# Kernel tuning notes

Measured on AMD Instinct MI355X. Metric: run time of the kernel, lower is better.

The kernel has to match this reference:

```python
import jax, jax.numpy as jnp
import numpy as np

B, N, E, T = 32768, 6, 6, 2  # batch graphs, nodes, edges (ring), edge types
H, DIN = 128, 3


def _ring_rel():
    # off_diag[i, (i+1)%N] = 1 -> edge e: sender i, receiver (i+1)%N
    send = np.arange(N)
    recv = (np.arange(N) + 1) % N
    eye = np.eye(N, dtype=np.float32)
    return jnp.asarray(eye[recv]), jnp.asarray(eye[send])  # rel_rec, rel_send [E,N]


def setup_inputs() -> dict:
    key = jax.random.key(0)
    ks = iter(jax.random.split(key, 40))
    rn = lambda shape, s=0.1: jax.random.normal(next(ks), shape, jnp.float32) * s
    rel_rec, rel_send = _ring_rel()
    inp = {
        'x': rn((B, N, DIN), 1.0),
        'rel_rec': rel_rec, 'rel_send': rel_send,
        'e1w1': rn((DIN, H)), 'e1b1': jnp.full((H,), 0.1), 'e1w2': rn((H, H)), 'e1b2': jnp.full((H,), 0.1),
        'e2w1': rn((2 * H, H)), 'e2b1': jnp.full((H,), 0.1), 'e2w2': rn((H, H)), 'e2b2': jnp.full((H,), 0.1),
        'e3w1': rn((H, H)), 'e3b1': jnp.full((H,), 0.1), 'e3w2': rn((H, H)), 'e3b2': jnp.full((H,), 0.1),
        'e4w1': rn((2 * H, H)), 'e4b1': jnp.full((H,), 0.1), 'e4w2': rn((H, H)), 'e4b2': jnp.full((H,), 0.1),
        'ew_out': rn((H, T)), 'eb_out': jnp.full((T,), 0.1),
        'd_msg_w1': rn((T, 2 * DIN, H)), 'd_msg_b1': rn((T, H), 0.01),
        'd_msg_w2': rn((T, H, H)), 'd_msg_b2': rn((T, H), 0.01),
        'd_out_w1': rn((DIN + H, H)), 'd_out_b1': rn((H,), 0.01),
        'd_out_w2': rn((H, H)), 'd_out_b2': rn((H,), 0.01),
        'd_out_w3': rn((H, DIN)), 'd_out_b3': rn((DIN,), 0.01),
    }
    return inp


def _mlp(h, w1, b1, w2, b2):
    # two-layer ELU MLP (dropout inactive at eval)
    return jax.nn.elu(jax.nn.elu(h @ w1 + b1) @ w2 + b2)


def reference(x, rel_rec, rel_send,
              e1w1, e1b1, e1w2, e1b2, e2w1, e2b1, e2w2, e2b2,
              e3w1, e3b1, e3w2, e3b2, e4w1, e4b1, e4w2, e4b2,
              ew_out, eb_out,
              d_msg_w1, d_msg_b1, d_msg_w2, d_msg_b2,
              d_out_w1, d_out_b1, d_out_w2, d_out_b2, d_out_w3, d_out_b3):
    node2edge = lambda h: jnp.concatenate(
        [jnp.einsum('en,bnh->beh', rel_rec, h), jnp.einsum('en,bnh->beh', rel_send, h)], axis=-1)

    # ---- GraphEncoder (factor=False) ----
    h = _mlp(x, e1w1, e1b1, e1w2, e1b2)                      # [B,N,H]
    he = _mlp(node2edge(h), e2w1, e2b1, e2w2, e2b2)          # [B,E,H]
    h2 = _mlp(he, e3w1, e3b1, e3w2, e3b2)                    # [B,E,H]
    h3 = _mlp(jnp.concatenate([h2, he], -1), e4w1, e4b1, e4w2, e4b2)
    logits = h3 @ ew_out + eb_out                            # [B,E,T]
    rel_type = jax.nn.softmax(logits, axis=-1)               # edge-type weights

    # ---- GraphDecoder single step (skip_first=False) ----
    recv = jnp.einsum('en,bnd->bed', rel_rec, x)             # [B,E,DIN]
    send = jnp.einsum('en,bnd->bed', rel_send, x)
    pre_msg = jnp.concatenate([recv, send], axis=-1)         # [B,E,2*DIN]
    # batched per-edge-type MLP: one grouped GEMM instead of a python loop of layers
    m = jax.nn.relu(jnp.einsum('bei,tih->bteh', pre_msg, d_msg_w1) + d_msg_b1[None, :, None, :])
    m = jax.nn.relu(jnp.einsum('bteh,tho->bteo', m, d_msg_w2) + d_msg_b2[None, :, None, :])
    all_msgs = jnp.einsum('bteh,bet->beh', m, rel_type)      # weight + accumulate over types
    agg_msgs = jnp.einsum('beh,en->bnh', all_msgs, rel_rec)  # edge -> node aggregation

    aug = jnp.concatenate([x, agg_msgs], axis=-1)            # [B,N,DIN+H]
    p = jax.nn.relu(aug @ d_out_w1 + d_out_b1)
    p = jax.nn.relu(p @ d_out_w2 + d_out_b2)
    p = p @ d_out_w3 + d_out_b3
    return x + p                                             # [B,N,DIN]
```

## Files before the change

kernel.cpp:

```cpp
#include <hip/hip_runtime.h>
#include <hip/hip_bf16.h>

typedef __bf16 bf16x8 __attribute__((ext_vector_type(8)));
typedef float floatx4 __attribute__((ext_vector_type(4)));

#define LDW 136
#define PXW 40

#define O_E1W2  0
#define O_E2W1  16384
#define O_E2W2  49152
#define O_E3W1  65536
#define O_E3W2  81920
#define O_E4W1  98304
#define O_E4W2  131072
#define O_DM2T0 147456
#define O_DM2T1 163840
#define O_DO1   180224
#define O_DO2   196608
#define O_EWOUT 212992
#define O_DW3   215040
#define O_E1W1P 217088
#define O_M1T0P 221184
#define O_M1T1P 225280
#define O_DO1XP 229376
#define WS_ELEMS 233472

__global__ void prep_kernel(const float* e1w2, const float* e2w1, const float* e2w2,
    const float* e3w1, const float* e3w2, const float* e4w1, const float* e4w2,
    const float* dmsg2, const float* dout1, const float* dout2,
    const float* ew_out, const float* dout_w3, const float* e1w1,
    const float* dmsg_w1, __hip_bfloat16* ws) {
  int idx = blockIdx.x * 256 + threadIdx.x;
  if (idx >= WS_ELEMS) return;
  float v;
  if (idx < O_E2W1)      { int l = idx;           v = e1w2[(l & 127) * 128 + (l >> 7)]; }
  else if (idx < O_E2W2) { int l = idx - O_E2W1;  v = e2w1[(l & 255) * 128 + (l >> 8)]; }
  else if (idx < O_E3W1) { int l = idx - O_E2W2;  v = e2w2[(l & 127) * 128 + (l >> 7)]; }
  else if (idx < O_E3W2) { int l = idx - O_E3W1;  v = e3w1[(l & 127) * 128 + (l >> 7)]; }
  else if (idx < O_E4W1) { int l = idx - O_E3W2;  v = e3w2[(l & 127) * 128 + (l >> 7)]; }
  else if (idx < O_E4W2) { int l = idx - O_E4W1;  v = e4w1[(l & 255) * 128 + (l >> 8)]; }
  else if (idx < O_DM2T0){ int l = idx - O_E4W2;  v = e4w2[(l & 127) * 128 + (l >> 7)]; }
  else if (idx < O_DM2T1){ int l = idx - O_DM2T0; v = dmsg2[(l & 127) * 128 + (l >> 7)]; }
  else if (idx < O_DO1)  { int l = idx - O_DM2T1; v = dmsg2[16384 + (l & 127) * 128 + (l >> 7)]; }
  else if (idx < O_DO2)  { int l = idx - O_DO1;   v = dout1[384 + (l & 127) * 128 + (l >> 7)]; }
  else if (idx < O_EWOUT){ int l = idx - O_DO2;   v = dout2[(l & 127) * 128 + (l >> 7)]; }
  else if (idx < O_DW3)  { int l = idx - O_EWOUT; int n = l >> 7;
                           v = (n < 2) ? ew_out[(l & 127) * 2 + n] : 0.f; }
  else if (idx < O_E1W1P){ int l = idx - O_DW3;   int n = l >> 7;
                           v = (n < 3) ? dout_w3[(l & 127) * 3 + n] : 0.f; }
  else if (idx < O_M1T0P){ int l = idx - O_E1W1P; int n = l >> 5, c = l & 31;
                           v = (c >= 3 && c < 6) ? e1w1[(c - 3) * 128 + n] : 0.f; }
  else if (idx < O_M1T1P){ int l = idx - O_M1T0P; int n = l >> 5, c = l & 31;
                           v = (c < 6) ? dmsg_w1[c * 128 + n] : 0.f; }
  else if (idx < O_DO1XP){ int l = idx - O_M1T1P; int n = l >> 5, c = l & 31;
                           v = (c < 6) ? dmsg_w1[768 + c * 128 + n] : 0.f; }
  else                   { int l = idx - O_DO1XP; int n = l >> 5, c = l & 31;
                           v = (c >= 3 && c < 6) ? dout1[(c - 3) * 128 + n] : 0.f; }
  ws[idx] = __float2bfloat16(v);
}

__global__ __launch_bounds__(512, 4) void nri_fused(
    const float* __restrict__ x,
    const float* __restrict__ e1b1, const float* __restrict__ e1b2,
    const float* __restrict__ e2b1, const float* __restrict__ e2b2,
    const float* __restrict__ e3b1, const float* __restrict__ e3b2,
    const float* __restrict__ e4b1, const float* __restrict__ e4b2,
    const float* __restrict__ eb_out,
    const float* __restrict__ dmsg_b1, const float* __restrict__ dmsg_b2,
    const float* __restrict__ dout_b1, const float* __restrict__ dout_b2,
    const float* __restrict__ dout_b3,
    const __bf16* __restrict__ wt, float* __restrict__ out)
{
  const int tid  = threadIdx.x;
  const int wave = tid >> 6;
  const int lane = tid & 63;
  const int nl   = lane & 15;
  const int quad = lane >> 4;
  const int colb = wave * 16 + nl;
  const int gx   = blockIdx.x * 288;

  __shared__ __align__(16) __hip_bfloat16 bufA[96 * LDW];
  __shared__ __align__(16) __hip_bfloat16 bufB[96 * LDW];
  __shared__ __align__(16) __hip_bfloat16 pxb[96 * PXW];
  __shared__ __align__(16) float biasL[16 * 128];
  __shared__ float rtw[192];
  __shared__ float xs[288];
  __shared__ float obuf[288];

  for (int i = tid; i < 288; i += 512) xs[i] = x[gx + i];
  for (int i = tid; i < 2048; i += 512) {
    int row = i >> 7, c = i & 127;
    float v;
    switch (row) {
      case 0: v = e1b1[c]; break;   case 1: v = e1b2[c]; break;
      case 2: v = e2b1[c]; break;   case 3: v = e2b2[c]; break;
      case 4: v = e3b1[c]; break;   case 5: v = e3b2[c]; break;
      case 6: v = e4b1[c]; break;   case 7: v = e4b2[c]; break;
      case 8: v = dmsg_b1[c]; break;  case 9: v = dmsg_b1[128 + c]; break;
      case 10: v = dmsg_b2[c]; break; case 11: v = dmsg_b2[128 + c]; break;
      case 12: v = dout_b1[c]; break; case 13: v = dout_b2[c]; break;
      case 14: v = (c < 2) ? eb_out[c] : 0.f; break;
      default: v = (c < 3) ? dout_b3[c] : 0.f; break;
    }
    biasL[i] = v;
  }
  for (int i = tid; i < 96 * 32; i += 512) {
    int row = i >> 5, c = i & 31;
    int e = row % 6;
    float v = 0.f;
    if (c < 3)      { int rr = row + ((e == 5) ? -5 : 1); v = x[gx + rr * 3 + c]; }
    else if (c < 6) v = x[gx + row * 3 + (c - 3)];
    pxb[row * PXW + c] = __float2bfloat16(v);
  }
  __syncthreads();

  auto initb = [&](floatx4 (&a)[6], int brow) {
    float bv = biasL[brow * 128 + colb];
    floatx4 v = {bv, bv, bv, bv};
#pragma unroll
    for (int mt = 0; mt < 6; ++mt) a[mt] = v;
  };

  auto gemm128 = [&](floatx4 (&acc)[6], const __hip_bfloat16* in, const __bf16* w) {
    const __bf16* ab = (const __bf16*)(const void*)in;
    const __bf16* w0 = w + colb * 128 + quad * 8;
#pragma unroll
    for (int ks = 0; ks < 4; ++ks) {
      int kk = ks * 32 + quad * 8;
      bf16x8 b0 = *(const bf16x8*)(w0 + ks * 32);
#pragma unroll
      for (int mt = 0; mt < 6; ++mt) {
        bf16x8 a = *(const bf16x8*)(ab + (mt * 16 + nl) * LDW + kk);
        acc[mt] = __builtin_amdgcn_mfma_f32_16x16x32_bf16(a, b0, acc[mt], 0, 0, 0);
      }
    }
  };

  auto gemm256 = [&](floatx4 (&acc)[6], const __hip_bfloat16* in0, bool recv0,
                     const __hip_bfloat16* in1, const __bf16* w) {
    int rofs0[6], rofs1[6];
#pragma unroll
    for (int mt = 0; mt < 6; ++mt) {
      int r = mt * 16 + nl;
      rofs1[mt] = r * LDW;
      if (recv0) { int e = r % 6; r += (e == 5) ? -5 : 1; }
      rofs0[mt] = r * LDW;
    }
    const __bf16* ab0 = (const __bf16*)(const void*)in0;
    const __bf16* ab1 = (const __bf16*)(const void*)in1;
    const __bf16* w0 = w + colb * 256 + quad * 8;
#pragma unroll
    for (int ks = 0; ks < 8; ++ks) {
      int kk = (ks & 3) * 32 + quad * 8;
      const __bf16* ab = (ks < 4) ? ab0 : ab1;
      const int* rofs = (ks < 4) ? rofs0 : rofs1;
      bf16x8 b0 = *(const bf16x8*)(w0 + ks * 32);
#pragma unroll
      for (int mt = 0; mt < 6; ++mt) {
        bf16x8 a = *(const bf16x8*)(ab + rofs[mt] + kk);
        acc[mt] = __builtin_amdgcn_mfma_f32_16x16x32_bf16(a, b0, acc[mt], 0, 0, 0);
      }
    }
  };

  auto gemm32 = [&](floatx4 (&acc)[6], int wofs) {
    const __bf16* pb = (const __bf16*)(const void*)pxb;
    bf16x8 b0 = *(const bf16x8*)(wt + wofs + colb * 32 + quad * 8);
#pragma unroll
    for (int mt = 0; mt < 6; ++mt) {
      bf16x8 a = *(const bf16x8*)(pb + (mt * 16 + nl) * PXW + quad * 8);
      acc[mt] = __builtin_amdgcn_mfma_f32_16x16x32_bf16(a, b0, acc[mt], 0, 0, 0);
    }
  };

  auto store_act = [&](floatx4 (&acc)[6], int act, __hip_bfloat16* ob) {
#pragma unroll
    for (int mt = 0; mt < 6; ++mt)
#pragma unroll
      for (int r = 0; r < 4; ++r) {
        float z = acc[mt][r];
        if (act == 1) z = (z > 0.f) ? z : (__expf(z) - 1.f);
        else z = fmaxf(z, 0.f);
        ob[(mt * 16 + quad * 4 + r) * LDW + colb] = __float2bfloat16(z);
      }
  };

  floatx4 acc[6];

  initb(acc, 0); gemm32(acc, O_E1W1P); store_act(acc, 1, bufA);
  __syncthreads();
  initb(acc, 1); gemm128(acc, bufA, wt + O_E1W2); store_act(acc, 1, bufB);
  __syncthreads();
  initb(acc, 2); gemm256(acc, bufB, true, bufB, wt + O_E2W1); store_act(acc, 1, bufA);
  __syncthreads();
  initb(acc, 3); gemm128(acc, bufA, wt + O_E2W2); store_act(acc, 1, bufB);
  __syncthreads();
  initb(acc, 4); gemm128(acc, bufB, wt + O_E3W1); store_act(acc, 1, bufA);
  __syncthreads();
  initb(acc, 5); gemm128(acc, bufA, wt + O_E3W2);
  __syncthreads();
  store_act(acc, 1, bufA);
  __syncthreads();
  initb(acc, 6); gemm256(acc, bufA, false, bufB, wt + O_E4W1);
  __syncthreads();
  store_act(acc, 1, bufA);
  __syncthreads();
  initb(acc, 7); gemm128(acc, bufA, wt + O_E4W2); store_act(acc, 1, bufB);
  __syncthreads();

  if (wave < 6) {
    int tile = wave;
    float bv = biasL[14 * 128 + nl];
    floatx4 lg = {bv, bv, bv, bv};
    const __bf16* ab = (const __bf16*)(const void*)bufB;
    const __bf16* wp = wt + O_EWOUT + nl * 128 + quad * 8;
#pragma unroll
    for (int ks = 0; ks < 4; ++ks) {
      bf16x8 a = *(const bf16x8*)(ab + (tile * 16 + nl) * LDW + ks * 32 + quad * 8);
      bf16x8 b = *(const bf16x8*)(wp + ks * 32);
      lg = __builtin_amdgcn_mfma_f32_16x16x32_bf16(a, b, lg, 0, 0, 0);
    }
    if (nl < 2) {
#pragma unroll
      for (int r = 0; r < 4; ++r)
        rtw[(tile * 16 + quad * 4 + r) * 2 + nl] = lg[r];
    }
  }
  __syncthreads();

  if (tid < 96) {
    float l0 = rtw[tid * 2], l1 = rtw[tid * 2 + 1];
    float mx = fmaxf(l0, l1);
    float ea = __expf(l0 - mx), eb = __expf(l1 - mx);
    float inv = 1.f / (ea + eb);
    rtw[tid * 2] = ea * inv; rtw[tid * 2 + 1] = eb * inv;
  }
  {
    floatx4 acc1[6];
    initb(acc, 8);  gemm32(acc, O_M1T0P);  store_act(acc, 2, bufA);
    initb(acc1, 9); gemm32(acc1, O_M1T1P); store_act(acc1, 2, bufB);
    __syncthreads();

    initb(acc, 10);  gemm128(acc, bufA, wt + O_DM2T0);
    initb(acc1, 11); gemm128(acc1, bufB, wt + O_DM2T1);
#pragma unroll
    for (int mt = 0; mt < 6; ++mt)
#pragma unroll
      for (int r = 0; r < 4; ++r) {
        int row = mt * 16 + quad * 4 + r;
        float r0 = rtw[row * 2], r1 = rtw[row * 2 + 1];
        acc[mt][r] = r0 * fmaxf(acc[mt][r], 0.f) + r1 * fmaxf(acc1[mt][r], 0.f);
      }
  }
  __syncthreads();

#pragma unroll
  for (int mt = 0; mt < 6; ++mt)
#pragma unroll
    for (int r = 0; r < 4; ++r) {
      int row = mt * 16 + quad * 4 + r;
      int e = row % 6;
      int orow = row + ((e == 5) ? -5 : 1);
      bufA[orow * LDW + colb] = __float2bfloat16(acc[mt][r]);
    }
  __syncthreads();

  initb(acc, 12); gemm128(acc, bufA, wt + O_DO1); gemm32(acc, O_DO1XP);
  store_act(acc, 2, bufB);
  __syncthreads();
  initb(acc, 13); gemm128(acc, bufB, wt + O_DO2); store_act(acc, 2, bufA);
  __syncthreads();

  if (wave < 6) {
    int tile = wave;
    float bv = biasL[15 * 128 + nl];
    floatx4 d = {bv, bv, bv, bv};
    const __bf16* ab = (const __bf16*)(const void*)bufA;
    const __bf16* wp = wt + O_DW3 + nl * 128 + quad * 8;
#pragma unroll
    for (int ks = 0; ks < 4; ++ks) {
      bf16x8 a = *(const bf16x8*)(ab + (tile * 16 + nl) * LDW + ks * 32 + quad * 8);
      bf16x8 b = *(const bf16x8*)(wp + ks * 32);
      d = __builtin_amdgcn_mfma_f32_16x16x32_bf16(a, b, d, 0, 0, 0);
    }
    if (nl < 3) {
#pragma unroll
      for (int r = 0; r < 4; ++r) {
        int row = tile * 16 + quad * 4 + r;
        obuf[row * 3 + nl] = xs[row * 3 + nl] + d[r];
      }
    }
  }
  __syncthreads();
  for (int i = tid; i < 288; i += 512) out[gx + i] = obuf[i];
}

extern "C" void kernel_launch(void* const* d_in, const int* in_sizes, int n_in,
                              void* d_out, int out_size, void* d_ws, size_t ws_size,
                              hipStream_t stream) {
  const float* x       = (const float*)d_in[0];
  const float* e1w1    = (const float*)d_in[3];
  const float* e1b1    = (const float*)d_in[4];
  const float* e1w2    = (const float*)d_in[5];
  const float* e1b2    = (const float*)d_in[6];
  const float* e2w1    = (const float*)d_in[7];
  const float* e2b1    = (const float*)d_in[8];
  const float* e2w2    = (const float*)d_in[9];
  const float* e2b2    = (const float*)d_in[10];
  const float* e3w1    = (const float*)d_in[11];
  const float* e3b1    = (const float*)d_in[12];
  const float* e3w2    = (const float*)d_in[13];
  const float* e3b2    = (const float*)d_in[14];
  const float* e4w1    = (const float*)d_in[15];
  const float* e4b1    = (const float*)d_in[16];
  const float* e4w2    = (const float*)d_in[17];
  const float* e4b2    = (const float*)d_in[18];
  const float* ew_out  = (const float*)d_in[19];
  const float* eb_out  = (const float*)d_in[20];
  const float* dmsg_w1 = (const float*)d_in[21];
  const float* dmsg_b1 = (const float*)d_in[22];
  const float* dmsg_w2 = (const float*)d_in[23];
  const float* dmsg_b2 = (const float*)d_in[24];
  const float* dout_w1 = (const float*)d_in[25];
  const float* dout_b1 = (const float*)d_in[26];
  const float* dout_w2 = (const float*)d_in[27];
  const float* dout_b2 = (const float*)d_in[28];
  const float* dout_w3 = (const float*)d_in[29];
  const float* dout_b3 = (const float*)d_in[30];

  prep_kernel<<<(WS_ELEMS + 255) / 256, 256, 0, stream>>>(
      e1w2, e2w1, e2w2, e3w1, e3w2, e4w1, e4w2, dmsg_w2, dout_w1, dout_w2,
      ew_out, dout_w3, e1w1, dmsg_w1, (__hip_bfloat16*)d_ws);

  nri_fused<<<32768 / 16, 512, 0, stream>>>(
      x, e1b1, e1b2, e2b1, e2b2, e3b1, e3b2, e4b1, e4b2, eb_out,
      dmsg_b1, dmsg_b2, dout_b1, dout_b2, dout_b3,
      (const __bf16*)d_ws, (float*)d_out);
}
```

Baseline: 276.7 us.

## Prefetch next-layer weights into registers and split e4w1 GEMM to overlap

Weight fragments for the next layer are loaded from global memory into registers before the current layer's activation store and barrier, so their latency overlaps other work instead of sitting inside the MFMA loop. The e4w1 256-wide GEMM is split into halves. The half that consumes the e2 output is fused with the e3w1 GEMM, which reads the same input buffer. This removes one extra barrier and store round trip but keeps a second accumulator set live, which raises VGPR pressure under launch_bounds(512,4) and risks spills.

```diff
diff --git a/kernel.cpp b/kernel.cpp
--- a/kernel.cpp
+++ b/kernel.cpp
@@ -60,6 +60,9 @@
   ws[idx] = __float2bfloat16(v);
 }
 
+struct W4 { bf16x8 b[4]; };
+struct W8 { bf16x8 b[8]; };
+
 __global__ __launch_bounds__(512, 4) void nri_fused(
     const float* __restrict__ x,
     const float* __restrict__ e1b1, const float* __restrict__ e1b2,
@@ -122,48 +125,75 @@
     for (int mt = 0; mt < 6; ++mt) a[mt] = v;
   };
 
-  auto gemm128 = [&](floatx4 (&acc)[6], const __hip_bfloat16* in, const __bf16* w) {
+  auto loadW128 = [&](int wofs) {
+    W4 w;
+    const __bf16* p = wt + wofs + colb * 128 + quad * 8;
+#pragma unroll
+    for (int ks = 0; ks < 4; ++ks) w.b[ks] = *(const bf16x8*)(p + ks * 32);
+    return w;
+  };
+  auto loadW256 = [&](int wofs) {
+    W8 w;
+    const __bf16* p = wt + wofs + colb * 256 + quad * 8;
+#pragma unroll
+    for (int ks = 0; ks < 8; ++ks) w.b[ks] = *(const bf16x8*)(p + ks * 32);
+    return w;
+  };
+  auto loadW256half = [&](int wofs, int kh) {
+    W4 w;
+    const __bf16* p = wt + wofs + colb * 256 + kh * 128 + quad * 8;
+#pragma unroll
+    for (int ks = 0; ks < 4; ++ks) w.b[ks] = *(const bf16x8*)(p + ks * 32);
+    return w;
+  };
+
+  auto gemmP = [&](floatx4 (&acc)[6], const W4& w, const __hip_bfloat16* in) {
     const __bf16* ab = (const __bf16*)(const void*)in;
-    const __bf16* w0 = w + colb * 128 + quad * 8;
 #pragma unroll
     for (int ks = 0; ks < 4; ++ks) {
       int kk = ks * 32 + quad * 8;
-      bf16x8 b0 = *(const bf16x8*)(w0 + ks * 32);
 #pragma unroll
       for (int mt = 0; mt < 6; ++mt) {
         bf16x8 a = *(const bf16x8*)(ab + (mt * 16 + nl) * LDW + kk);
-        acc[mt] = __builtin_amdgcn_mfma_f32_16x16x32_bf16(a, b0, acc[mt], 0, 0, 0);
-      }
-    }
-  };
-
-  auto gemm256 = [&](floatx4 (&acc)[6], const __hip_bfloat16* in0, bool recv0,
-                     const __hip_bfloat16* in1, const __bf16* w) {
+        acc[mt] = __builtin_amdgcn_mfma_f32_16x16x32_bf16(a, w.b[ks], acc[mt], 0, 0, 0);
+      }
+    }
+  };
+  auto gemmP2 = [&](floatx4 (&accA)[6], const W4& wA, floatx4 (&accB)[6],
+                    const W4& wB, const __hip_bfloat16* in) {
+    const __bf16* ab = (const __bf16*)(const void*)in;
+#pragma unroll
+    for (int ks = 0; ks < 4; ++ks) {
+      int kk = ks * 32 + quad * 8;
+#pragma unroll
+      for (int mt = 0; mt < 6; ++mt) {
+        bf16x8 a = *(const bf16x8*)(ab + (mt * 16 + nl) * LDW + kk);
+        accA[mt] = __builtin_amdgcn_mfma_f32_16x16x32_bf16(a, wA.b[ks], accA[mt], 0, 0, 0);
+        accB[mt] = __builtin_amdgcn_mfma_f32_16x16x32_bf16(a, wB.b[ks], accB[mt], 0, 0, 0);
+      }
+    }
+  };
+  auto gemm256P = [&](floatx4 (&acc)[6], const W8& w, const __hip_bfloat16* in) {
     int rofs0[6], rofs1[6];
 #pragma unroll
     for (int mt = 0; mt < 6; ++mt) {
       int r = mt * 16 + nl;
       rofs1[mt] = r * LDW;
-      if (recv0) { int e = r % 6; r += (e == 5) ? -5 : 1; }
-      rofs0[mt] = r * LDW;
-    }
-    const __bf16* ab0 = (const __bf16*)(const void*)in0;
-    const __bf16* ab1 = (const __bf16*)(const void*)in1;
-    const __bf16* w0 = w + colb * 256 + quad * 8;
+      int e = r % 6;
+      rofs0[mt] = (r + ((e == 5) ? -5 : 1)) * LDW;
+    }
+    const __bf16* ab = (const __bf16*)(const void*)in;
 #pragma unroll
     for (int ks = 0; ks < 8; ++ks) {
       int kk = (ks & 3) * 32 + quad * 8;
-      const __bf16* ab = (ks < 4) ? ab0 : ab1;
       const int* rofs = (ks < 4) ? rofs0 : rofs1;
-      bf16x8 b0 = *(const bf16x8*)(w0 + ks * 32);
 #pragma unroll
       for (int mt = 0; mt < 6; ++mt) {
         bf16x8 a = *(const bf16x8*)(ab + rofs[mt] + kk);
-        acc[mt] = __builtin_amdgcn_mfma_f32_16x16x32_bf16(a, b0, acc[mt], 0, 0, 0);
-      }
-    }
-  };
-
+        acc[mt] = __builtin_amdgcn_mfma_f32_16x16x32_bf16(a, w.b[ks], acc[mt], 0, 0, 0);
+      }
+    }
+  };
   auto gemm32 = [&](floatx4 (&acc)[6], int wofs) {
     const __bf16* pb = (const __bf16*)(const void*)pxb;
     bf16x8 b0 = *(const bf16x8*)(wt + wofs + colb * 32 + quad * 8);
@@ -173,7 +203,6 @@
       acc[mt] = __builtin_amdgcn_mfma_f32_16x16x32_bf16(a, b0, acc[mt], 0, 0, 0);
     }
   };
-
   auto store_act = [&](floatx4 (&acc)[6], int act, __hip_bfloat16* ob) {
 #pragma unroll
     for (int mt = 0; mt < 6; ++mt)
@@ -186,27 +215,40 @@
       }
   };
 
-  floatx4 acc[6];
-
-  initb(acc, 0); gemm32(acc, O_E1W1P); store_act(acc, 1, bufA);
-  __syncthreads();
-  initb(acc, 1); gemm128(acc, bufA, wt + O_E1W2); store_act(acc, 1, bufB);
-  __syncthreads();
-  initb(acc, 2); gemm256(acc, bufB, true, bufB, wt + O_E2W1); store_act(acc, 1, bufA);
-  __syncthreads();
-  initb(acc, 3); gemm128(acc, bufA, wt + O_E2W2); store_act(acc, 1, bufB);
-  __syncthreads();
-  initb(acc, 4); gemm128(acc, bufB, wt + O_E3W1); store_act(acc, 1, bufA);
-  __syncthreads();
-  initb(acc, 5); gemm128(acc, bufA, wt + O_E3W2);
-  __syncthreads();
+  floatx4 acc[6], acc2[6];
+
+  initb(acc, 0); gemm32(acc, O_E1W1P);
+  W4 w2 = loadW128(O_E1W2);
   store_act(acc, 1, bufA);
   __syncthreads();
-  initb(acc, 6); gemm256(acc, bufA, false, bufB, wt + O_E4W1);
-  __syncthreads();
+  initb(acc, 1); gemmP(acc, w2, bufA);
+  W8 w3 = loadW256(O_E2W1);
+  store_act(acc, 1, bufB);
+  __syncthreads();
+  initb(acc, 2); gemm256P(acc, w3, bufB);
+  W4 w4 = loadW128(O_E2W2);
   store_act(acc, 1, bufA);
   __syncthreads();
-  initb(acc, 7); gemm128(acc, bufA, wt + O_E4W2); store_act(acc, 1, bufB);
+  initb(acc, 3); gemmP(acc, w4, bufA);
+  W4 w5 = loadW128(O_E3W1);
+  W4 w5b = loadW256half(O_E4W1, 1);
+  store_act(acc, 1, bufB);
+  __syncthreads();
+  initb(acc, 4); initb(acc2, 6);
+  gemmP2(acc, w5, acc2, w5b, bufB);
+  W4 w6 = loadW128(O_E3W2);
+  store_act(acc, 1, bufA);
+  __syncthreads();
+  initb(acc, 5); gemmP(acc, w6, bufA);
+  W4 w7 = loadW256half(O_E4W1, 0);
+  store_act(acc, 1, bufB);
+  __syncthreads();
+  gemmP(acc2, w7, bufB);
+  W4 w8 = loadW128(O_E4W2);
+  store_act(acc2, 1, bufA);
+  __syncthreads();
+  initb(acc, 7); gemmP(acc, w8, bufA);
+  store_act(acc, 1, bufB);
   __syncthreads();
 
   if (wave < 6) {
@@ -236,23 +278,23 @@
     float inv = 1.f / (ea + eb);
     rtw[tid * 2] = ea * inv; rtw[tid * 2 + 1] = eb * inv;
   }
-  {
-    floatx4 acc1[6];
-    initb(acc, 8);  gemm32(acc, O_M1T0P);  store_act(acc, 2, bufA);
-    initb(acc1, 9); gemm32(acc1, O_M1T1P); store_act(acc1, 2, bufB);
-    __syncthreads();
-
-    initb(acc, 10);  gemm128(acc, bufA, wt + O_DM2T0);
-    initb(acc1, 11); gemm128(acc1, bufB, wt + O_DM2T1);
-#pragma unroll
-    for (int mt = 0; mt < 6; ++mt)
-#pragma unroll
-      for (int r = 0; r < 4; ++r) {
-        int row = mt * 16 + quad * 4 + r;
-        float r0 = rtw[row * 2], r1 = rtw[row * 2 + 1];
-        acc[mt][r] = r0 * fmaxf(acc[mt][r], 0.f) + r1 * fmaxf(acc1[mt][r], 0.f);
-      }
-  }
+  initb(acc, 8);  gemm32(acc, O_M1T0P);  store_act(acc, 2, bufA);
+  initb(acc2, 9); gemm32(acc2, O_M1T1P); store_act(acc2, 2, bufB);
+  W4 wm0 = loadW128(O_DM2T0);
+  W4 wm1 = loadW128(O_DM2T1);
+  __syncthreads();
+
+  initb(acc, 10);  gemmP(acc, wm0, bufA);
+  initb(acc2, 11); gemmP(acc2, wm1, bufB);
+#pragma unroll
+  for (int mt = 0; mt < 6; ++mt)
+#pragma unroll
+    for (int r = 0; r < 4; ++r) {
+      int row = mt * 16 + quad * 4 + r;
+      float r0 = rtw[row * 2], r1 = rtw[row * 2 + 1];
+      acc[mt][r] = r0 * fmaxf(acc[mt][r], 0.f) + r1 * fmaxf(acc2[mt][r], 0.f);
+    }
+  W4 wd1 = loadW128(O_DO1);
   __syncthreads();
 
 #pragma unroll
@@ -266,10 +308,12 @@
     }
   __syncthreads();
 
-  initb(acc, 12); gemm128(acc, bufA, wt + O_DO1); gemm32(acc, O_DO1XP);
+  initb(acc, 12); gemmP(acc, wd1, bufA); gemm32(acc, O_DO1XP);
+  W4 wd2 = loadW128(O_DO2);
   store_act(acc, 2, bufB);
   __syncthreads();
-  initb(acc, 13); gemm128(acc, bufB, wt + O_DO2); store_act(acc, 2, bufA);
+  initb(acc, 13); gemmP(acc, wd2, bufB);
+  store_act(acc, 2, bufA);
   __syncthreads();
 
   if (wave < 6) {
```

Measured after the change: 267.1 us. 3.5% less time.
